# Optimization experiments

Measured on AMD Instinct MI355X. Metric: run time of the kernel, lower is better.

## Reference

```python
import jax, jax.numpy as jnp
import numpy as np
from jax import lax

NX, NG = 128, 64
P = NX * NG            # 8192
T = 4                  # timesteps in the walk
N_ITER = 50            # attractor iterations
KAPPA, LAMDA, YITA = 0.8, 0.9, 0.1
NEG_SLOPE = 0.01       # torch LeakyReLU default


def f_p(v):
    # LeakyReLU(clamp(v, -1, 1))
    c = jnp.clip(v, -1.0, 1.0)
    return jnp.where(c >= 0, c, NEG_SLOPE * c)


def setup_inputs() -> dict:
    key = jax.random.key(0)
    k1, k2, k3 = jax.random.split(key, 3)
    x = jax.random.uniform(k1, (T, NX), dtype=jnp.float32)
    g = jax.random.uniform(k2, (T, NG), dtype=jnp.float32)
    # small random initial memory so the attractor dynamics are non-trivial
    M0 = 0.01 * jax.random.normal(k3, (P, P), dtype=jnp.float32)
    return {"x": x, "g": g, "M0": M0}


def reference(x, g, M0):
    # W_tile = kron(ones(1, nx), eye(ng)) : [ng, P]; g @ W_tile tiles g nx times
    W_tile = jnp.kron(jnp.ones((1, NX), jnp.float32), jnp.eye(NG, dtype=jnp.float32))

    def step(M, xg):
        xt, gt = xg                      # [NX], [NG]
        query = gt @ W_tile              # [P]
        h0 = f_p(query)

        def inner(h, _):
            # hop_type == 1: h = f_p(kappa*h + h * (h @ M))
            h = f_p(KAPPA * h + h * (h @ M))
            return h, None

        h, _ = lax.scan(inner, h0, None, length=N_ITER)   # attractor retrieval p_
        p = (xt[:, None] * gt[None, :]).reshape(P)        # p = outer(x, g).ravel()
        loss = jnp.sum(jnp.abs(p - h))
        # heb_type == 0: M = lamda*M + yita * outer(p + p_, p - p_)
        M = LAMDA * M + YITA * jnp.outer(p + h, p - h)
        return M, loss

    M_final, losses = lax.scan(step, M0, (x, g))
    return jnp.sum(losses)
```

## Files before the change

kernel.cpp:

```cpp
#include <hip/hip_runtime.h>

constexpr int PP = 8192;
constexpr int NGc = 64;
constexpr int NXc = 128;
constexpr float KAPPA = 0.8f;
constexpr float NEG   = 0.01f;

constexpr int CHUNKS = 256;
constexpr int ROWSB  = PP / CHUNKS;
constexpr int PV     = PP / 4;

__device__ __forceinline__ float f_p(float v) {
    float c = fminf(fmaxf(v, -1.0f), 1.0f);
    return c >= 0.0f ? c : NEG * c;
}
__device__ __forceinline__ float bl(unsigned u) { return __uint_as_float(u << 16); }
__device__ __forceinline__ float bh(unsigned u) { return __uint_as_float(u & 0xffff0000u); }
__device__ __forceinline__ unsigned pack_bf16(float lo, float hi) {
    unsigned a = __float_as_uint(lo), b = __float_as_uint(hi);
    a = (a + 0x7fffu + ((a >> 16) & 1u)) >> 16;
    b = (b + 0x7fffu + ((b >> 16) & 1u)) & 0xffff0000u;
    return a | b;
}

__global__ void k_convert(const float4* __restrict__ M4, uint4* __restrict__ Mb) {
    size_t idx = (size_t)blockIdx.x * 256 + threadIdx.x;
    float4 a = M4[2 * idx], b = M4[2 * idx + 1];
    uint4 o;
    o.x = pack_bf16(a.x, a.y); o.y = pack_bf16(a.z, a.w);
    o.z = pack_bf16(b.x, b.y); o.w = pack_bf16(b.z, b.w);
    Mb[idx] = o;
}

__global__ void k_init(float* __restrict__ h, const float* __restrict__ g,
                       const float* __restrict__ u, float* __restrict__ dots0, int t) {
    int c = blockIdx.x * 256 + threadIdx.x;
    float h0 = f_p(g[c & (NGc - 1)]);
    h[c] = h0;
    if (t > 0) {
        __shared__ float red[3][4];
        float pd[3];
        pd[0] = h0 * u[c];
        pd[1] = (t > 1) ? h0 * u[PP + c] : 0.f;
        pd[2] = (t > 2) ? h0 * u[2 * PP + c] : 0.f;
        #pragma unroll
        for (int k = 0; k < 3; ++k) {
            float s = pd[k];
            #pragma unroll
            for (int off = 32; off > 0; off >>= 1) s += __shfl_down(s, off);
            if ((threadIdx.x & 63) == 0) red[k][threadIdx.x >> 6] = s;
        }
        __syncthreads();
        if (threadIdx.x == 0) {
            #pragma unroll
            for (int k = 0; k < 3; ++k)
                if (k < t) atomicAdd(&dots0[k], red[k][0] + red[k][1] + red[k][2] + red[k][3]);
        }
    }
}

__global__ void k_matvec_bf16(const uint4* __restrict__ Mb, const float* __restrict__ h,
                              float4* __restrict__ ybuf4, float* __restrict__ dzero) {
    if (dzero && blockIdx.x == 0 && blockIdx.y == 0 && threadIdx.x < 4)
        dzero[threadIdx.x] = 0.f;
    __shared__ float hs[ROWSB];
    int i0 = blockIdx.y * ROWSB;
    if (threadIdx.x < ROWSB) hs[threadIdx.x] = h[i0 + threadIdx.x];
    __syncthreads();
    int c8 = blockIdx.x * 512 + threadIdx.x;
    const uint4* Mp = Mb + (size_t)i0 * 1024 + c8;
    float a0=0,a1=0,a2=0,a3=0,a4=0,a5=0,a6=0,a7=0;
    #pragma unroll 8
    for (int r = 0; r < ROWSB; ++r) {
        uint4 m = Mp[(size_t)r * 1024];
        float hv = hs[r];
        a0 += hv * bl(m.x); a1 += hv * bh(m.x);
        a2 += hv * bl(m.y); a3 += hv * bh(m.y);
        a4 += hv * bl(m.z); a5 += hv * bh(m.z);
        a6 += hv * bl(m.w); a7 += hv * bh(m.w);
    }
    size_t base = (size_t)blockIdx.y * PV + (size_t)c8 * 2;
    ybuf4[base]     = make_float4(a0, a1, a2, a3);
    ybuf4[base + 1] = make_float4(a4, a5, a6, a7);
}

__global__ void k_matvec_f32(const float4* __restrict__ M4, const float* __restrict__ h,
                             float4* __restrict__ ybuf4, float* __restrict__ dzero) {
    if (dzero && blockIdx.x == 0 && blockIdx.y == 0 && threadIdx.x < 4)
        dzero[threadIdx.x] = 0.f;
    __shared__ float hs[ROWSB];
    int i0 = blockIdx.y * ROWSB;
    if (threadIdx.x < ROWSB) hs[threadIdx.x] = h[i0 + threadIdx.x];
    __syncthreads();
    int c4 = blockIdx.x * 512 + threadIdx.x;
    const float4* Mp = M4 + (size_t)i0 * PV + c4;
    float4 acc = {0.f, 0.f, 0.f, 0.f};
    #pragma unroll 8
    for (int r = 0; r < ROWSB; ++r) {
        float4 m = Mp[(size_t)r * PV];
        float hv = hs[r];
        acc.x += hv * m.x; acc.y += hv * m.y;
        acc.z += hv * m.z; acc.w += hv * m.w;
    }
    ybuf4[(size_t)blockIdx.y * PV + c4] = acc;
}

__global__ void k_update(float* __restrict__ h, const float4* __restrict__ ybuf4,
                         const float4* __restrict__ u4, const float4* __restrict__ v4,
                         const float* __restrict__ dR, float* __restrict__ dW,
                         float lt, float c0, float c1, float c2, int t) {
    int tid = threadIdx.x;
    int jv  = blockIdx.x * 16 + (tid & 15);
    int cl  = tid >> 4;
    float4 s = {0.f, 0.f, 0.f, 0.f};
    #pragma unroll
    for (int c = 0; c < CHUNKS / 32; ++c) {
        float4 m = ybuf4[(size_t)(cl * (CHUNKS / 32) + c) * PV + jv];
        s.x += m.x; s.y += m.y; s.z += m.z; s.w += m.w;
    }
    __shared__ float4 red[512];
    red[tid] = s;
    __syncthreads();
    for (int off = 256; off >= 16; off >>= 1) {
        if (tid < off) {
            float4 o = red[tid + off];
            red[tid].x += o.x; red[tid].y += o.y;
            red[tid].z += o.z; red[tid].w += o.w;
        }
        __syncthreads();
    }
    if (tid < 16) {
        int j4 = blockIdx.x * 16 + tid;
        float4 z = red[tid];
        z.x *= lt; z.y *= lt; z.z *= lt; z.w *= lt;
        if (t > 0) {
            float w0 = c0 * dR[0];
            float4 vv = v4[j4];
            z.x += w0 * vv.x; z.y += w0 * vv.y; z.z += w0 * vv.z; z.w += w0 * vv.w;
        }
        if (t > 1) {
            float w1 = c1 * dR[1];
            float4 vv = v4[PV + j4];
            z.x += w1 * vv.x; z.y += w1 * vv.y; z.z += w1 * vv.z; z.w += w1 * vv.w;
        }
        if (t > 2) {
            float w2 = c2 * dR[2];
            float4 vv = v4[2 * PV + j4];
            z.x += w2 * vv.x; z.y += w2 * vv.y; z.z += w2 * vv.z; z.w += w2 * vv.w;
        }
        float4* h4 = (float4*)h;
        float4 hv = h4[j4];
        float4 hn;
        hn.x = f_p(KAPPA * hv.x + hv.x * z.x);
        hn.y = f_p(KAPPA * hv.y + hv.y * z.y);
        hn.z = f_p(KAPPA * hv.z + hv.z * z.z);
        hn.w = f_p(KAPPA * hv.w + hv.w * z.w);
        h4[j4] = hn;
        if (t > 0) {
            float pd[3] = {0.f, 0.f, 0.f};
            #pragma unroll
            for (int k = 0; k < 3; ++k) {
                if (k < t) {
                    float4 uk = u4[(size_t)k * PV + j4];
                    pd[k] = hn.x * uk.x + hn.y * uk.y + hn.z * uk.z + hn.w * uk.w;
                }
            }
            #pragma unroll
            for (int off = 8; off > 0; off >>= 1) {
                pd[0] += __shfl_down(pd[0], off);
                pd[1] += __shfl_down(pd[1], off);
                pd[2] += __shfl_down(pd[2], off);
            }
            if (tid == 0) {
                #pragma unroll
                for (int k = 0; k < 3; ++k)
                    if (k < t) atomicAdd(&dW[k], pd[k]);
            }
        }
    }
}

__global__ void k_epilogue(const float* __restrict__ h, const float* __restrict__ x,
                           const float* __restrict__ g, float* __restrict__ u,
                           float* __restrict__ v, float* __restrict__ loss,
                           float* __restrict__ dbase) {
    int c = blockIdx.x * 256 + threadIdx.x;
    if (blockIdx.x == 0 && threadIdx.x < 12) dbase[threadIdx.x] = 0.f;
    float p = x[c >> 6] * g[c & (NGc - 1)];
    float hc = h[c];
    float d = p - hc;
    u[c] = p + hc;
    v[c] = d;
    float a = fabsf(d);
    __shared__ float red[4];
    #pragma unroll
    for (int off = 32; off > 0; off >>= 1) a += __shfl_down(a, off);
    if ((threadIdx.x & 63) == 0) red[threadIdx.x >> 6] = a;
    __syncthreads();
    if (threadIdx.x == 0)
        atomicAdd(loss, red[0] + red[1] + red[2] + red[3]);
}

extern "C" void kernel_launch(void* const* d_in, const int* in_sizes, int n_in,
                              void* d_out, int out_size, void* d_ws, size_t ws_size,
                              hipStream_t stream) {
    const float* x  = (const float*)d_in[0];
    const float* g  = (const float*)d_in[1];
    const float* M0 = (const float*)d_in[2];

    const size_t MB_BYTES   = (size_t)PP * PP * 2;
    const size_t YBUF_BYTES = (size_t)CHUNKS * PP * 4;
    const size_t SMALL      = PP * 4 + 2 * 4 * PP * 4 + 256;
    bool useBf16 = ws_size >= MB_BYTES + YBUF_BYTES + SMALL;

    char* ws = (char*)d_ws;
    uint4* Mb = nullptr;
    if (useBf16) { Mb = (uint4*)ws; ws += MB_BYTES; }
    float* ybuf = (float*)ws;  ws += YBUF_BYTES;
    float* h    = (float*)ws;  ws += PP * 4;
    float* u    = (float*)ws;  ws += 4 * PP * 4;
    float* v    = (float*)ws;  ws += 4 * PP * 4;
    float* dbase = (float*)ws;

    hipMemsetAsync(d_out, 0, sizeof(float), stream);
    if (useBf16)
        k_convert<<<(PP / 8) * (PP / 256), 256, 0, stream>>>((const float4*)M0, Mb);

    const float lts[4] = {1.0f, 0.9f, 0.81f, 0.729f};
    const float C0[4]  = {0.f, 0.1f, 0.09f, 0.081f};
    const float C1[4]  = {0.f, 0.f,  0.1f,  0.09f};
    const float C2[4]  = {0.f, 0.f,  0.f,   0.1f};

    for (int t = 0; t < 4; ++t) {
        k_init<<<PP / 256, 256, 0, stream>>>(h, g + t * NGc, u, dbase, t);
        for (int it = 0; it < 50; ++it) {
            float* dz = (t > 0) ? dbase + 4 * ((it + 1) % 3) : nullptr;
            float* dR = dbase + 4 * (it % 3);
            float* dW = dbase + 4 * ((it + 1) % 3);
            if (useBf16)
                k_matvec_bf16<<<dim3(2, CHUNKS), 512, 0, stream>>>(Mb, h, (float4*)ybuf, dz);
            else
                k_matvec_f32<<<dim3(4, CHUNKS), 512, 0, stream>>>((const float4*)M0, h, (float4*)ybuf, dz);
            k_update<<<128, 512, 0, stream>>>(h, (const float4*)ybuf, (const float4*)u,
                                              (const float4*)v, dR, dW,
                                              lts[t], C0[t], C1[t], C2[t], t);
        }
        k_epilogue<<<PP / 256, 256, 0, stream>>>(h, x + t * NXc, g + t * NGc,
                                                 u + (size_t)t * PP, v + (size_t)t * PP,
                                                 (float*)d_out, dbase);
    }
}
```

Before: 6.651 ms.

## Convert as many matrix rows to bf16 as workspace allows, rest stay f32

```diff
diff --git a/kernel.cpp b/kernel.cpp
--- a/kernel.cpp
+++ b/kernel.cpp
@@ -6,7 +6,7 @@
 constexpr float KAPPA = 0.8f;
 constexpr float NEG   = 0.01f;
 
-constexpr int CHUNKS = 256;
+constexpr int CHUNKS = 128;
 constexpr int ROWSB  = PP / CHUNKS;
 constexpr int PV     = PP / 4;
 
@@ -59,33 +59,9 @@
     }
 }
 
-__global__ void k_matvec_bf16(const uint4* __restrict__ Mb, const float* __restrict__ h,
-                              float4* __restrict__ ybuf4, float* __restrict__ dzero) {
-    if (dzero && blockIdx.x == 0 && blockIdx.y == 0 && threadIdx.x < 4)
-        dzero[threadIdx.x] = 0.f;
-    __shared__ float hs[ROWSB];
-    int i0 = blockIdx.y * ROWSB;
-    if (threadIdx.x < ROWSB) hs[threadIdx.x] = h[i0 + threadIdx.x];
-    __syncthreads();
-    int c8 = blockIdx.x * 512 + threadIdx.x;
-    const uint4* Mp = Mb + (size_t)i0 * 1024 + c8;
-    float a0=0,a1=0,a2=0,a3=0,a4=0,a5=0,a6=0,a7=0;
-    #pragma unroll 8
-    for (int r = 0; r < ROWSB; ++r) {
-        uint4 m = Mp[(size_t)r * 1024];
-        float hv = hs[r];
-        a0 += hv * bl(m.x); a1 += hv * bh(m.x);
-        a2 += hv * bl(m.y); a3 += hv * bh(m.y);
-        a4 += hv * bl(m.z); a5 += hv * bh(m.z);
-        a6 += hv * bl(m.w); a7 += hv * bh(m.w);
-    }
-    size_t base = (size_t)blockIdx.y * PV + (size_t)c8 * 2;
-    ybuf4[base]     = make_float4(a0, a1, a2, a3);
-    ybuf4[base + 1] = make_float4(a4, a5, a6, a7);
-}
-
-__global__ void k_matvec_f32(const float4* __restrict__ M4, const float* __restrict__ h,
-                             float4* __restrict__ ybuf4, float* __restrict__ dzero) {
+__global__ void k_matvec(const uint2* __restrict__ Mb, const float4* __restrict__ M4,
+                         const float* __restrict__ h, float4* __restrict__ ybuf4,
+                         float* __restrict__ dzero, int Rrows) {
     if (dzero && blockIdx.x == 0 && blockIdx.y == 0 && threadIdx.x < 4)
         dzero[threadIdx.x] = 0.f;
     __shared__ float hs[ROWSB];
@@ -93,14 +69,25 @@
     if (threadIdx.x < ROWSB) hs[threadIdx.x] = h[i0 + threadIdx.x];
     __syncthreads();
     int c4 = blockIdx.x * 512 + threadIdx.x;
-    const float4* Mp = M4 + (size_t)i0 * PV + c4;
     float4 acc = {0.f, 0.f, 0.f, 0.f};
-    #pragma unroll 8
-    for (int r = 0; r < ROWSB; ++r) {
-        float4 m = Mp[(size_t)r * PV];
-        float hv = hs[r];
-        acc.x += hv * m.x; acc.y += hv * m.y;
-        acc.z += hv * m.z; acc.w += hv * m.w;
+    if (i0 < Rrows) {
+        const uint2* Mp = Mb + (size_t)i0 * PV + c4;
+        #pragma unroll 8
+        for (int r = 0; r < ROWSB; ++r) {
+            uint2 m = Mp[(size_t)r * PV];
+            float hv = hs[r];
+            acc.x += hv * bl(m.x); acc.y += hv * bh(m.x);
+            acc.z += hv * bl(m.y); acc.w += hv * bh(m.y);
+        }
+    } else {
+        const float4* Mp = M4 + (size_t)i0 * PV + c4;
+        #pragma unroll 8
+        for (int r = 0; r < ROWSB; ++r) {
+            float4 m = Mp[(size_t)r * PV];
+            float hv = hs[r];
+            acc.x += hv * m.x; acc.y += hv * m.y;
+            acc.z += hv * m.z; acc.w += hv * m.w;
+        }
     }
     ybuf4[(size_t)blockIdx.y * PV + c4] = acc;
 }
@@ -208,14 +195,16 @@
     const float* g  = (const float*)d_in[1];
     const float* M0 = (const float*)d_in[2];
 
-    const size_t MB_BYTES   = (size_t)PP * PP * 2;
     const size_t YBUF_BYTES = (size_t)CHUNKS * PP * 4;
     const size_t SMALL      = PP * 4 + 2 * 4 * PP * 4 + 256;
-    bool useBf16 = ws_size >= MB_BYTES + YBUF_BYTES + SMALL;
+
+    size_t avail = (ws_size > YBUF_BYTES + SMALL) ? ws_size - YBUF_BYTES - SMALL : 0;
+    long long Rl = (long long)(avail / ((size_t)PP * 2));
+    int R = (int)(Rl > PP ? PP : Rl);
+    R &= ~(ROWSB - 1);
 
     char* ws = (char*)d_ws;
-    uint4* Mb = nullptr;
-    if (useBf16) { Mb = (uint4*)ws; ws += MB_BYTES; }
+    uint2* Mb = (uint2*)ws;    ws += (size_t)R * PP * 2;
     float* ybuf = (float*)ws;  ws += YBUF_BYTES;
     float* h    = (float*)ws;  ws += PP * 4;
     float* u    = (float*)ws;  ws += 4 * PP * 4;
@@ -223,8 +212,8 @@
     float* dbase = (float*)ws;
 
     hipMemsetAsync(d_out, 0, sizeof(float), stream);
-    if (useBf16)
-        k_convert<<<(PP / 8) * (PP / 256), 256, 0, stream>>>((const float4*)M0, Mb);
+    if (R > 0)
+        k_convert<<<R * (PP / 8) / 256, 256, 0, stream>>>((const float4*)M0, (uint4*)Mb);
 
     const float lts[4] = {1.0f, 0.9f, 0.81f, 0.729f};
     const float C0[4]  = {0.f, 0.1f, 0.09f, 0.081f};
@@ -237,10 +226,8 @@
             float* dz = (t > 0) ? dbase + 4 * ((it + 1) % 3) : nullptr;
             float* dR = dbase + 4 * (it % 3);
             float* dW = dbase + 4 * ((it + 1) % 3);
-            if (useBf16)
-                k_matvec_bf16<<<dim3(2, CHUNKS), 512, 0, stream>>>(Mb, h, (float4*)ybuf, dz);
-            else
-                k_matvec_f32<<<dim3(4, CHUNKS), 512, 0, stream>>>((const float4*)M0, h, (float4*)ybuf, dz);
+            k_matvec<<<dim3(4, CHUNKS), 512, 0, stream>>>(
+                Mb, (const float4*)M0, h, (float4*)ybuf, dz, R);
             k_update<<<128, 512, 0, stream>>>(h, (const float4*)ybuf, (const float4*)u,
                                               (const float4*)v, dR, dW,
                                               lts[t], C0[t], C1[t], C2[t], t);
```

New measurement: 6.013 ms. 9.6% less time.
